# Optimization experiments

Hardware: AMD Instinct MI355X
Metric: run time of the kernel (lower is better)

The kernel has to match this reference:

```python
import jax, jax.numpy as jnp
import numpy as np

NUM_HEADS = 12
LN_EPS = 1e-5


def _ln(x, g, b):
    m = x.mean(-1, keepdims=True)
    v = ((x - m) ** 2).mean(-1, keepdims=True)
    return (x - m) * jax.lax.rsqrt(v + LN_EPS) * g + b


def _attn(q, k, v):
    sim = jnp.einsum('bid,bjd->bij', q, k)
    a = jax.nn.softmax(sim, axis=-1)
    return jnp.einsum('bij,bjd->bid', a, v)


def _var_attn(x, qkv_w, qkv_b, proj_w, proj_b, f, n, mode):
    # Faithful port of VarAttention.forward_features (num_tokens=0, pt_att=True)
    B, N, D = x.shape
    h = NUM_HEADS
    hd = D // h
    qkv = x @ qkv_w + qkv_b                       # [B, N, 3D]
    q, k, v = jnp.split(qkv, 3, axis=-1)

    def heads(t):  # 'b n (h d) -> (b h) n d'
        return t.reshape(B, N, h, hd).transpose(0, 2, 1, 3).reshape(B * h, N, hd)

    q = heads(q) * (hd ** -0.5)
    k = heads(k)
    v = heads(v)
    BH = B * h
    cls_q, q_ = q[:, :1], q[:, 1:]
    cls_k, k_ = k[:, :1], k[:, 1:]
    cls_v, v_ = v[:, :1], v[:, 1:]
    cls_out = _attn(cls_q, k, v)                  # cls attends over ALL tokens

    if mode == 'time':  # 'b (f n) d -> (b n) f d'
        to = lambda t: t.reshape(BH, f, n, hd).transpose(0, 2, 1, 3).reshape(BH * n, f, hd)
        back = lambda t: t.reshape(BH, n, f, hd).transpose(0, 2, 1, 3).reshape(BH, f * n, hd)
        r = n
    else:               # 'b (f n) d -> (b f) n d'
        to = lambda t: t.reshape(BH * f, n, hd)
        back = lambda t: t.reshape(BH, f * n, hd)
        r = f

    q_, k_, v_ = to(q_), to(k_), to(v_)
    cls_k_r = jnp.broadcast_to(cls_k[:, None], (BH, r, 1, hd)).reshape(BH * r, 1, hd)
    cls_v_r = jnp.broadcast_to(cls_v[:, None], (BH, r, 1, hd)).reshape(BH * r, 1, hd)
    out = _attn(q_, jnp.concatenate([cls_k_r, k_], axis=1),
                jnp.concatenate([cls_v_r, v_], axis=1))
    out = jnp.concatenate([cls_out, back(out)], axis=1)   # [(B h), N, d]
    out = out.reshape(B, h, N, hd).transpose(0, 2, 1, 3).reshape(B, N, D)
    return out @ proj_w + proj_b


def setup_inputs() -> dict:
    key = jax.random.key(0)
    ks = jax.random.split(key, 8)
    B, F, n, D = 8, 8, 196, 768
    N = 1 + F * n
    s = 0.02
    return {
        'x': jax.random.normal(ks[0], (B, N, D), jnp.float32),
        'norm1_g': jnp.ones((D,), jnp.float32), 'norm1_b': jnp.zeros((D,), jnp.float32),
        'norm2_g': jnp.ones((D,), jnp.float32), 'norm2_b': jnp.zeros((D,), jnp.float32),
        'norm3_g': jnp.ones((D,), jnp.float32), 'norm3_b': jnp.zeros((D,), jnp.float32),
        'attn_qkv_w': jax.random.normal(ks[1], (D, 3 * D), jnp.float32) * s,
        'attn_qkv_b': jnp.zeros((3 * D,), jnp.float32),
        'attn_proj_w': jax.random.normal(ks[2], (D, D), jnp.float32) * s,
        'attn_proj_b': jnp.zeros((D,), jnp.float32),
        'time_qkv_w': jax.random.normal(ks[3], (D, 3 * D), jnp.float32) * s,
        'time_qkv_b': jnp.zeros((3 * D,), jnp.float32),
        'time_proj_w': jax.random.normal(ks[4], (D, D), jnp.float32) * s,
        'time_proj_b': jnp.zeros((D,), jnp.float32),
        'fc1_w': jax.random.normal(ks[5], (D, 4 * D), jnp.float32) * s,
        'fc1_b': jnp.zeros((4 * D,), jnp.float32),
        'fc2_w': jax.random.normal(ks[6], (4 * D, D), jnp.float32) * s,
        'fc2_b': jnp.zeros((D,), jnp.float32),
        'f': 8,
    }


def reference(x, norm1_g, norm1_b, norm2_g, norm2_b, norm3_g, norm3_b,
              attn_qkv_w, attn_qkv_b, attn_proj_w, attn_proj_b,
              time_qkv_w, time_qkv_b, time_proj_w, time_proj_b,
              fc1_w, fc1_b, fc2_w, fc2_b, f):
    N = x.shape[1]
    n = (N - 1) // f  # patches per frame
    # divided time attention
    time_out = _var_attn(_ln(x, norm3_g, norm3_b), time_qkv_w, time_qkv_b,
                         time_proj_w, time_proj_b, f, n, 'time')
    time_residual = x + time_out
    # divided space attention (frozen-in-time: residual from original x)
    space_out = _var_attn(_ln(time_residual, norm1_g, norm1_b), attn_qkv_w, attn_qkv_b,
                          attn_proj_w, attn_proj_b, f, n, 'space')
    space_residual = x + space_out
    # MLP with exact GELU (torch nn.GELU default)
    h = jax.nn.gelu(_ln(space_residual, norm2_g, norm2_b) @ fc1_w + fc1_b, approximate=False)
    return space_residual + (h @ fc2_w + fc2_b)
```

## Files before the change

### kernel.cpp

```cpp
#include <hip/hip_runtime.h>
#include <hip/hip_bf16.h>
#include <math.h>

#define DM    768
#define NH    12
#define HD    64
#define BB    8
#define FF    8
#define NP    196
#define NT    1569
#define MROWS 12552
#define MPAD  12672
#define YT    99
#define QKVN  2304
#define FCN   3072
#define CHK   197

typedef short s16;
typedef __attribute__((ext_vector_type(8))) short short8;
typedef __attribute__((ext_vector_type(4))) float floatx4;

__device__ __forceinline__ float bf2f(s16 s) {
  union { unsigned u; float f; } x;
  x.u = ((unsigned)(unsigned short)s) << 16;
  return x.f;
}
__device__ __forceinline__ s16 f2bf(float f) {
  __hip_bfloat16 h = __float2bfloat16(f);
  s16 r;
  __builtin_memcpy(&r, &h, sizeof(r));
  return r;
}
__device__ __forceinline__ void gload16(const void* g, void* l) {
  __builtin_amdgcn_global_load_lds(
      (__attribute__((address_space(1))) void*)g,
      (__attribute__((address_space(3))) void*)l, 16, 0, 0);
}

__global__ void wtrans(const float* __restrict__ W, s16* __restrict__ Wt,
                       int K, int Nn) {
  __shared__ float t[32][33];
  int n0 = blockIdx.x * 32, k0 = blockIdx.y * 32;
  int tx = threadIdx.x, ty = threadIdx.y;
#pragma unroll
  for (int i = 0; i < 4; ++i)
    t[ty + 8*i][tx] = W[(size_t)(k0 + ty + 8*i) * Nn + n0 + tx];
  __syncthreads();
#pragma unroll
  for (int i = 0; i < 4; ++i)
    Wt[(size_t)(n0 + ty + 8*i) * K + k0 + tx] = f2bf(t[tx][ty + 8*i]);
}

__global__ __launch_bounds__(256) void ln_k(const float* __restrict__ in,
                                            const float* __restrict__ g,
                                            const float* __restrict__ b,
                                            s16* __restrict__ out) {
  __shared__ float red[8];
  int row = blockIdx.x;
  int tid = threadIdx.x;
  const float* rp = in + (size_t)row * DM;
  float v0 = rp[tid], v1 = rp[tid + 256], v2 = rp[tid + 512];
  float s = v0 + v1 + v2;
#pragma unroll
  for (int o = 32; o; o >>= 1) s += __shfl_down(s, o);
  if ((tid & 63) == 0) red[tid >> 6] = s;
  __syncthreads();
  float mean = (red[0] + red[1] + red[2] + red[3]) * (1.0f / DM);
  __syncthreads();
  float d0 = v0 - mean, d1 = v1 - mean, d2 = v2 - mean;
  float q = d0*d0 + d1*d1 + d2*d2;
#pragma unroll
  for (int o = 32; o; o >>= 1) q += __shfl_down(q, o);
  if ((tid & 63) == 0) red[tid >> 6] = q;
  __syncthreads();
  float var = (red[0] + red[1] + red[2] + red[3]) * (1.0f / DM);
  float rs = rsqrtf(var + 1e-5f);
  s16* op = out + (size_t)row * DM;
  op[tid      ] = f2bf(d0 * rs * g[tid      ] + b[tid      ]);
  op[tid + 256] = f2bf(d1 * rs * g[tid + 256] + b[tid + 256]);
  op[tid + 512] = f2bf(d2 * rs * g[tid + 512] + b[tid + 512]);
}

template<int EPI>
__global__ __launch_bounds__(256, 3) void gemm128(const s16* __restrict__ A,
                                                  const s16* __restrict__ Bt,
                                                  const float* __restrict__ bias,
                                                  const float* __restrict__ resid,
                                                  void* __restrict__ out,
                                                  int K, int Nn, int xt) {
  __shared__ s16 As0[128 * 32], As1[128 * 32];
  __shared__ s16 Bs0[128 * 32], Bs1[128 * 32];
  const int nwg = gridDim.x, orig = blockIdx.x;
  const int qq = nwg >> 3, rr = nwg & 7, xcd = orig & 7, lid = orig >> 3;
  const int wgid = (xcd < rr ? xcd * (qq + 1) : rr * (qq + 1) + (xcd - rr) * qq) + lid;
  const int row0 = (wgid / xt) * 128, col0 = (wgid % xt) * 128;
  const int tid = threadIdx.x;
  const int wave = tid >> 6, lane = tid & 63;
  const int wr = wave >> 1, wc = wave & 1;
  const int lrow = lane & 15, lk = (lane >> 4) * 8;

  floatx4 acc[4][4] = {};

  for (int k0 = 0; k0 < K; k0 += 64) {
#pragma unroll
    for (int i = 0; i < 2; ++i) {
      int elem = ((i * 4 + wave) << 9) + (lane << 3);
      int r = elem >> 5, c = elem & 31;
      const s16* Ap = A  + (size_t)(row0 + r) * K + k0 + c;
      const s16* Bp = Bt + (size_t)(col0 + r) * K + k0 + c;
      gload16(Ap,      As0 + elem);
      gload16(Ap + 32, As1 + elem);
      gload16(Bp,      Bs0 + elem);
      gload16(Bp + 32, Bs1 + elem);
    }
    __syncthreads();
    short8 af0[4], af1[4], bf0[4], bf1[4];
#pragma unroll
    for (int mi = 0; mi < 4; ++mi) {
      int ro = ((wr * 64 + mi * 16 + lrow) << 5) + lk;
      af0[mi] = *reinterpret_cast<const short8*>(As0 + ro);
      af1[mi] = *reinterpret_cast<const short8*>(As1 + ro);
    }
#pragma unroll
    for (int ni = 0; ni < 4; ++ni) {
      int ro = ((wc * 64 + ni * 16 + lrow) << 5) + lk;
      bf0[ni] = *reinterpret_cast<const short8*>(Bs0 + ro);
      bf1[ni] = *reinterpret_cast<const short8*>(Bs1 + ro);
    }
#pragma unroll
    for (int mi = 0; mi < 4; ++mi)
#pragma unroll
      for (int ni = 0; ni < 4; ++ni) {
        acc[mi][ni] = __builtin_amdgcn_mfma_f32_16x16x32_bf16(af0[mi], bf0[ni], acc[mi][ni], 0, 0, 0);
        acc[mi][ni] = __builtin_amdgcn_mfma_f32_16x16x32_bf16(af1[mi], bf1[ni], acc[mi][ni], 0, 0, 0);
      }
    __syncthreads();
  }

  const int c_lane = lane & 15, r_lane = lane >> 4;
#pragma unroll
  for (int mi = 0; mi < 4; ++mi) {
#pragma unroll
    for (int j = 0; j < 4; ++j) {
      int r = row0 + wr * 64 + mi * 16 + r_lane * 4 + j;
      if (r >= MROWS) continue;
#pragma unroll
      for (int ni = 0; ni < 4; ++ni) {
        int c = col0 + wc * 64 + ni * 16 + c_lane;
        float v = acc[mi][ni][j] + bias[c];
        size_t idx = (size_t)r * Nn + c;
        if (EPI == 0) {
          ((s16*)out)[idx] = f2bf(v);
        } else if (EPI == 1) {
          float ge = 0.5f * v * (1.0f + erff(v * 0.70710678118654752f));
          ((s16*)out)[idx] = f2bf(ge);
        } else {
          ((float*)out)[idx] = resid[idx] + v;
        }
      }
    }
  }
}

__global__ __launch_bounds__(256) void cls_part(const s16* __restrict__ qkv,
                                                float* __restrict__ part) {
  __shared__ float qs[64];
  __shared__ float sc[CHK];
  __shared__ float pacc[4][64];
  __shared__ float red[8];
  int blk = blockIdx.x; int ch = blk & 7; int bh = blk >> 3;
  int b = bh / NH, h = bh % NH;
  int tid = threadIdx.x;
  int t0 = ch * CHK;
  int nk = NT - t0; if (nk > CHK) nk = CHK;
  if (tid < 64) qs[tid] = 0.125f * bf2f(qkv[(size_t)(b*NT) * QKVN + h*HD + tid]);
  __syncthreads();
  for (int i = tid; i < nk; i += 256) {
    const s16* kp = qkv + (size_t)(b*NT + t0 + i) * QKVN + DM + h*HD;
    float dot = 0.f;
#pragma unroll
    for (int d8 = 0; d8 < 8; ++d8) {
      short8 kv = *reinterpret_cast<const short8*>(kp + d8*8);
#pragma unroll
      for (int j = 0; j < 8; ++j) dot += qs[d8*8 + j] * bf2f(kv[j]);
    }
    sc[i] = dot;
  }
  __syncthreads();
  float m = -1e30f;
  for (int i = tid; i < nk; i += 256) m = fmaxf(m, sc[i]);
#pragma unroll
  for (int o = 32; o; o >>= 1) m = fmaxf(m, __shfl_xor(m, o));
  if ((tid & 63) == 0) red[tid >> 6] = m;
  __syncthreads();
  m = fmaxf(fmaxf(red[0], red[1]), fmaxf(red[2], red[3]));
  __syncthreads();
  float s = 0.f;
  for (int i = tid; i < nk; i += 256) { float e = __expf(sc[i] - m); sc[i] = e; s += e; }
#pragma unroll
  for (int o = 32; o; o >>= 1) s += __shfl_xor(s, o);
  if ((tid & 63) == 0) red[tid >> 6] = s;
  __syncthreads();
  float S = red[0] + red[1] + red[2] + red[3];
  int d = tid & 63, pt = tid >> 6;
  float a = 0.f;
  for (int i = pt; i < nk; i += 4)
    a += sc[i] * bf2f(qkv[(size_t)(b*NT + t0 + i) * QKVN + 2*DM + h*HD + d]);
  pacc[pt][d] = a;
  __syncthreads();
  float* pp = part + (size_t)blk * 66;
  if (tid < 64) pp[2 + tid] = pacc[0][tid] + pacc[1][tid] + pacc[2][tid] + pacc[3][tid];
  if (tid == 0) { pp[0] = m; pp[1] = S; }
}

__global__ __launch_bounds__(64) void cls_combine(const float* __restrict__ part,
                                                  s16* __restrict__ aout) {
  int bh = blockIdx.x; int b = bh / NH, h = bh % NH;
  int d = threadIdx.x;
  float m = -1e30f;
#pragma unroll
  for (int c = 0; c < 8; ++c) m = fmaxf(m, part[(size_t)(bh*8 + c) * 66]);
  float S = 0.f, A = 0.f;
#pragma unroll
  for (int c = 0; c < 8; ++c) {
    const float* pp = part + (size_t)(bh*8 + c) * 66;
    float w = __expf(pp[0] - m);
    S += pp[1] * w;
    A += w * pp[2 + d];
  }
  aout[(size_t)(b*NT) * DM + h*HD + d] = f2bf(A / S);
}

__global__ __launch_bounds__(256) void time_attn(const s16* __restrict__ qkv,
                                                 s16* __restrict__ aout) {
  int g = blockIdx.x * 4 + (threadIdx.x >> 6);
  int lane = threadIdx.x & 63;
  int p = g % NP; int bh = g / NP; int b = bh / NH, h = bh % NH;
  int qi = lane >> 3;
  int dc = (lane & 7) * 8;
  int tokq = 1 + qi*NP + p;
  short8 qv = *reinterpret_cast<const short8*>(qkv + (size_t)(b*NT + tokq)*QKVN + h*HD + dc);
  float qf[8];
#pragma unroll
  for (int j = 0; j < 8; ++j) qf[j] = 0.125f * bf2f(qv[j]);
  float s[9];
#pragma unroll
  for (int kj = 0; kj < 9; ++kj) {
    int tok = (kj == 0) ? 0 : (1 + (kj - 1)*NP + p);
    short8 kv = *reinterpret_cast<const short8*>(qkv + (size_t)(b*NT + tok)*QKVN + DM + h*HD + dc);
    float d = 0.f;
#pragma unroll
    for (int j = 0; j < 8; ++j) d += qf[j] * bf2f(kv[j]);
    d += __shfl_xor(d, 1); d += __shfl_xor(d, 2); d += __shfl_xor(d, 4);
    s[kj] = d;
  }
  float m = s[0];
#pragma unroll
  for (int kj = 1; kj < 9; ++kj) m = fmaxf(m, s[kj]);
  float sum = 0.f;
#pragma unroll
  for (int kj = 0; kj < 9; ++kj) { s[kj] = expf(s[kj] - m); sum += s[kj]; }
  float inv = 1.0f / sum;
  float o[8] = {0,0,0,0,0,0,0,0};
#pragma unroll
  for (int kj = 0; kj < 9; ++kj) {
    int tok = (kj == 0) ? 0 : (1 + (kj - 1)*NP + p);
    short8 vv = *reinterpret_cast<const short8*>(qkv + (size_t)(b*NT + tok)*QKVN + 2*DM + h*HD + dc);
#pragma unroll
    for (int j = 0; j < 8; ++j) o[j] += s[kj] * bf2f(vv[j]);
  }
  short8 ov;
#pragma unroll
  for (int j = 0; j < 8; ++j) ov[j] = f2bf(o[j] * inv);
  *reinterpret_cast<short8*>(aout + (size_t)(b*NT + tokq)*DM + h*HD + dc) = ov;
}

#define PST 232
#define VST 232
__global__ __launch_bounds__(256) void space_attn_mfma(const s16* __restrict__ qkv,
                                                       s16* __restrict__ aout) {
  __shared__ s16 Vt[64][VST];
  __shared__ s16 P[4][16][PST];
  int grp = blockIdx.x;
  int fr = grp & 7; int bh = grp >> 3; int b = bh / NH, h = bh % NH;
  int tid = threadIdx.x, w = tid >> 6, lane = tid & 63;
  const size_t hbase = (size_t)(b * NT) * QKVN + h * HD;

  for (int idx = tid; idx < 224 * 8; idx += 256) {
    int kj = idx >> 3, c8 = idx & 7;
    if (kj < 197) {
      int tok = (kj == 0) ? 0 : (1 + fr * NP + kj - 1);
      short8 vv = *reinterpret_cast<const short8*>(qkv + hbase + (size_t)tok * QKVN + 2 * DM + c8 * 8);
#pragma unroll
      for (int j = 0; j < 8; ++j) Vt[c8 * 8 + j][kj] = vv[j];
    } else {
#pragma unroll
      for (int j = 0; j < 8; ++j) Vt[c8 * 8 + j][kj] = 0;
    }
  }
  for (int i = tid; i < 4 * 16 * 16; i += 256) {
    int wv = i >> 8, rr2 = (i >> 4) & 15, cc = i & 15;
    P[wv][rr2][208 + cc] = 0;
  }
  __syncthreads();

  const int lr = lane & 15, lg = lane >> 4;

  for (int t0 = w; t0 < 13; t0 += 4) {
    int q0 = t0 * 16;
    short8 aq[2];
#pragma unroll
    for (int c = 0; c < 2; ++c) {
      int tokq = 1 + fr * NP + q0 + lr;
      aq[c] = *reinterpret_cast<const short8*>(qkv + hbase + (size_t)tokq * QKVN + c * 32 + lg * 8);
    }
    short8 kb[13][2];
#pragma unroll
    for (int t = 0; t < 13; ++t) {
#pragma unroll
      for (int c = 0; c < 2; ++c) {
        int krow = t * 16 + lr;
        int tokk = (krow == 0) ? 0 : (1 + fr * NP + krow - 1);
        kb[t][c] = *reinterpret_cast<const short8*>(qkv + hbase + (size_t)tokk * QKVN + DM + c * 32 + lg * 8);
      }
    }
    floatx4 st[13];
#pragma unroll
    for (int t = 0; t < 13; ++t) st[t] = (floatx4){0.f, 0.f, 0.f, 0.f};
#pragma unroll
    for (int t = 0; t < 13; ++t) {
      st[t] = __builtin_amdgcn_mfma_f32_16x16x32_bf16(aq[0], kb[t][0], st[t], 0, 0, 0);
      st[t] = __builtin_amdgcn_mfma_f32_16x16x32_bf16(aq[1], kb[t][1], st[t], 0, 0, 0);
    }
    float mj[4] = {-1e30f, -1e30f, -1e30f, -1e30f};
#pragma unroll
    for (int t = 0; t < 13; ++t) {
      int key = t * 16 + lr;
#pragma unroll
      for (int j = 0; j < 4; ++j) {
        float v = (key < 197) ? st[t][j] * 0.125f : -1e30f;
        st[t][j] = v;
        mj[j] = fmaxf(mj[j], v);
      }
    }
#pragma unroll
    for (int j = 0; j < 4; ++j) {
      mj[j] = fmaxf(mj[j], __shfl_xor(mj[j], 1));
      mj[j] = fmaxf(mj[j], __shfl_xor(mj[j], 2));
      mj[j] = fmaxf(mj[j], __shfl_xor(mj[j], 4));
      mj[j] = fmaxf(mj[j], __shfl_xor(mj[j], 8));
    }
    float su[4] = {0.f, 0.f, 0.f, 0.f};
#pragma unroll
    for (int t = 0; t < 13; ++t)
#pragma unroll
      for (int j = 0; j < 4; ++j) {
        float e = __expf(st[t][j] - mj[j]);
        st[t][j] = e;
        su[j] += e;
      }
#pragma unroll
    for (int j = 0; j < 4; ++j) {
      su[j] += __shfl_xor(su[j], 1);
      su[j] += __shfl_xor(su[j], 2);
      su[j] += __shfl_xor(su[j], 4);
      su[j] += __shfl_xor(su[j], 8);
    }
    float inv[4];
#pragma unroll
    for (int j = 0; j < 4; ++j) inv[j] = 1.0f / su[j];
#pragma unroll
    for (int t = 0; t < 13; ++t)
#pragma unroll
      for (int j = 0; j < 4; ++j)
        P[w][lg * 4 + j][t * 16 + lr] = f2bf(st[t][j]);
    floatx4 o[4];
#pragma unroll
    for (int dt = 0; dt < 4; ++dt) o[dt] = (floatx4){0.f, 0.f, 0.f, 0.f};
#pragma unroll
    for (int kc = 0; kc < 7; ++kc) {
      short8 pa = *reinterpret_cast<const short8*>(&P[w][lr][kc * 32 + lg * 8]);
#pragma unroll
      for (int dt = 0; dt < 4; ++dt) {
        short8 vb = *reinterpret_cast<const short8*>(&Vt[dt * 16 + lr][kc * 32 + lg * 8]);
        o[dt] = __builtin_amdgcn_mfma_f32_16x16x32_bf16(pa, vb, o[dt], 0, 0, 0);
      }
    }
#pragma unroll
    for (int dt = 0; dt < 4; ++dt)
#pragma unroll
      for (int j = 0; j < 4; ++j) {
        int q = q0 + lg * 4 + j;
        if (q < NP) {
          int tokq = 1 + fr * NP + q;
          aout[(size_t)(b * NT + tokq) * DM + h * HD + dt * 16 + lr] = f2bf(o[dt][j] * inv[j]);
        }
      }
  }
}

extern "C" void kernel_launch(void* const* d_in, const int* in_sizes, int n_in,
                              void* d_out, int out_size, void* d_ws, size_t ws_size,
                              hipStream_t stream) {
  const float* x       = (const float*)d_in[0];
  const float* n1g     = (const float*)d_in[1];
  const float* n1b     = (const float*)d_in[2];
  const float* n2g     = (const float*)d_in[3];
  const float* n2b     = (const float*)d_in[4];
  const float* n3g     = (const float*)d_in[5];
  const float* n3b     = (const float*)d_in[6];
  const float* aqkv_w  = (const float*)d_in[7];
  const float* aqkv_b  = (const float*)d_in[8];
  const float* aproj_w = (const float*)d_in[9];
  const float* aproj_b = (const float*)d_in[10];
  const float* tqkv_w  = (const float*)d_in[11];
  const float* tqkv_b  = (const float*)d_in[12];
  const float* tproj_w = (const float*)d_in[13];
  const float* tproj_b = (const float*)d_in[14];
  const float* fc1_w   = (const float*)d_in[15];
  const float* fc1_b   = (const float*)d_in[16];
  const float* fc2_w   = (const float*)d_in[17];
  const float* fc2_b   = (const float*)d_in[18];
  float* out = (float*)d_out;

  char* ws = (char*)d_ws;
  size_t off = 0;
  auto alloc = [&](size_t bytes) -> void* {
    void* p = ws + off;
    off += (bytes + 255) & ~(size_t)255;
    return p;
  };
  s16*  wt_tqkv  = (s16*)alloc((size_t)QKVN * DM * 2);
  s16*  wt_tproj = (s16*)alloc((size_t)DM * DM * 2);
  s16*  wt_aqkv  = (s16*)alloc((size_t)QKVN * DM * 2);
  s16*  wt_aproj = (s16*)alloc((size_t)DM * DM * 2);
  s16*  wt_fc1   = (s16*)alloc((size_t)FCN * DM * 2);
  s16*  wt_fc2   = (s16*)alloc((size_t)DM * FCN * 2);
  s16*  ln_out   = (s16*)alloc((size_t)MPAD * DM * 2);
  s16*  attnout  = (s16*)alloc((size_t)MPAD * DM * 2);
  float* resid_s = (float*)alloc((size_t)MROWS * DM * 4);
  float* clspart = (float*)alloc((size_t)BB * NH * 8 * 66 * 4);
  char* big      = (char*)alloc((size_t)MPAD * FCN * 2);
  s16*   qkv_buf = (s16*)big;
  float* resid_t = (float*)big;
  s16*   h_buf   = (s16*)big;

  dim3 tb(32, 8);
  wtrans<<<dim3(QKVN/32, DM/32), tb, 0, stream>>>(tqkv_w,  wt_tqkv,  DM, QKVN);
  wtrans<<<dim3(DM/32,   DM/32), tb, 0, stream>>>(tproj_w, wt_tproj, DM, DM);
  wtrans<<<dim3(QKVN/32, DM/32), tb, 0, stream>>>(aqkv_w,  wt_aqkv,  DM, QKVN);
  wtrans<<<dim3(DM/32,   DM/32), tb, 0, stream>>>(aproj_w, wt_aproj, DM, DM);
  wtrans<<<dim3(FCN/32,  DM/32), tb, 0, stream>>>(fc1_w,   wt_fc1,   DM, FCN);
  wtrans<<<dim3(DM/32,  FCN/32), tb, 0, stream>>>(fc2_w,   wt_fc2,   FCN, DM);

  const int XT_QKV = QKVN / 128, XT_PRJ = DM / 128, XT_FC1 = FCN / 128;

  ln_k<<<MROWS, 256, 0, stream>>>(x, n3g, n3b, ln_out);
  gemm128<0><<<XT_QKV * YT, 256, 0, stream>>>(ln_out, wt_tqkv, tqkv_b, nullptr, qkv_buf, DM, QKVN, XT_QKV);
  cls_part<<<BB*NH*8, 256, 0, stream>>>(qkv_buf, clspart);
  cls_combine<<<BB*NH, 64, 0, stream>>>(clspart, attnout);
  time_attn<<<(BB*NH*NP)/4, 256, 0, stream>>>(qkv_buf, attnout);
  gemm128<2><<<XT_PRJ * YT, 256, 0, stream>>>(attnout, wt_tproj, tproj_b, x, resid_t, DM, DM, XT_PRJ);

  ln_k<<<MROWS, 256, 0, stream>>>(resid_t, n1g, n1b, ln_out);
  gemm128<0><<<XT_QKV * YT, 256, 0, stream>>>(ln_out, wt_aqkv, aqkv_b, nullptr, qkv_buf, DM, QKVN, XT_QKV);
  cls_part<<<BB*NH*8, 256, 0, stream>>>(qkv_buf, clspart);
  cls_combine<<<BB*NH, 64, 0, stream>>>(clspart, attnout);
  space_attn_mfma<<<BB*NH*FF, 256, 0, stream>>>(qkv_buf, attnout);
  gemm128<2><<<XT_PRJ * YT, 256, 0, stream>>>(attnout, wt_aproj, aproj_b, x, resid_s, DM, DM, XT_PRJ);

  ln_k<<<MROWS, 256, 0, stream>>>(resid_s, n2g, n2b, ln_out);
  gemm128<1><<<XT_FC1 * YT, 256, 0, stream>>>(ln_out, wt_fc1, fc1_b, nullptr, h_buf, DM, FCN, XT_FC1);
  gemm128<2><<<XT_PRJ * YT, 256, 0, stream>>>(h_buf, wt_fc2, fc2_b, resid_s, out, FCN, DM, XT_PRJ);
}
```

Measured before the change: 651.5 us.

## Double-buffer GEMM shared memory tiles to overlap global loads with MFMA

The bf16 GEMM kernel now keeps two LDS stages and issues the global-to-LDS loads for the next K tile before computing on the current one, with one barrier per iteration. This is meant to hide global load latency behind the MFMA work. LDS per block doubles to 64KB and launch bounds drop from 3 to 2 blocks per CU, so occupancy falls. Whether the loads actually overlap depends on how gload16 waits on completion.

```diff
diff --git a/kernel.cpp b/kernel.cpp
--- a/kernel.cpp
+++ b/kernel.cpp
@@ -82,14 +82,14 @@
 }
 
 template<int EPI>
-__global__ __launch_bounds__(256, 3) void gemm128(const s16* __restrict__ A,
+__global__ __launch_bounds__(256, 2) void gemm128(const s16* __restrict__ A,
                                                   const s16* __restrict__ Bt,
                                                   const float* __restrict__ bias,
                                                   const float* __restrict__ resid,
                                                   void* __restrict__ out,
                                                   int K, int Nn, int xt) {
-  __shared__ s16 As0[128 * 32], As1[128 * 32];
-  __shared__ s16 Bs0[128 * 32], Bs1[128 * 32];
+  __shared__ s16 As[2][2][128 * 32];
+  __shared__ s16 Bs[2][2][128 * 32];
   const int nwg = gridDim.x, orig = blockIdx.x;
   const int qq = nwg >> 3, rr = nwg & 7, xcd = orig & 7, lid = orig >> 3;
   const int wgid = (xcd < rr ? xcd * (qq + 1) : rr * (qq + 1) + (xcd - rr) * qq) + lid;
@@ -98,34 +98,44 @@
   const int wave = tid >> 6, lane = tid & 63;
   const int wr = wave >> 1, wc = wave & 1;
   const int lrow = lane & 15, lk = (lane >> 4) * 8;
+  const int nt = K >> 6;
+
+#define STAGE(kt_, cur_)                                                       \
+  {                                                                            \
+    int k0s = (kt_) * 64;                                                      \
+    _Pragma("unroll")                                                          \
+    for (int i = 0; i < 2; ++i) {                                              \
+      int elem = ((i * 4 + wave) << 9) + (lane << 3);                          \
+      int r = elem >> 5, c = elem & 31;                                        \
+      const s16* Ap = A  + (size_t)(row0 + r) * K + k0s + c;                   \
+      const s16* Bp = Bt + (size_t)(col0 + r) * K + k0s + c;                   \
+      gload16(Ap,      As[cur_][0] + elem);                                    \
+      gload16(Ap + 32, As[cur_][1] + elem);                                    \
+      gload16(Bp,      Bs[cur_][0] + elem);                                    \
+      gload16(Bp + 32, Bs[cur_][1] + elem);                                    \
+    }                                                                          \
+  }
 
   floatx4 acc[4][4] = {};
 
-  for (int k0 = 0; k0 < K; k0 += 64) {
-#pragma unroll
-    for (int i = 0; i < 2; ++i) {
-      int elem = ((i * 4 + wave) << 9) + (lane << 3);
-      int r = elem >> 5, c = elem & 31;
-      const s16* Ap = A  + (size_t)(row0 + r) * K + k0 + c;
-      const s16* Bp = Bt + (size_t)(col0 + r) * K + k0 + c;
-      gload16(Ap,      As0 + elem);
-      gload16(Ap + 32, As1 + elem);
-      gload16(Bp,      Bs0 + elem);
-      gload16(Bp + 32, Bs1 + elem);
-    }
-    __syncthreads();
+  STAGE(0, 0)
+  __syncthreads();
+
+  int cur = 0;
+  for (int kt = 0; kt < nt; ++kt) {
+    if (kt + 1 < nt) STAGE(kt + 1, cur ^ 1)
     short8 af0[4], af1[4], bf0[4], bf1[4];
 #pragma unroll
     for (int mi = 0; mi < 4; ++mi) {
       int ro = ((wr * 64 + mi * 16 + lrow) << 5) + lk;
-      af0[mi] = *reinterpret_cast<const short8*>(As0 + ro);
-      af1[mi] = *reinterpret_cast<const short8*>(As1 + ro);
+      af0[mi] = *reinterpret_cast<const short8*>(As[cur][0] + ro);
+      af1[mi] = *reinterpret_cast<const short8*>(As[cur][1] + ro);
     }
 #pragma unroll
     for (int ni = 0; ni < 4; ++ni) {
       int ro = ((wc * 64 + ni * 16 + lrow) << 5) + lk;
-      bf0[ni] = *reinterpret_cast<const short8*>(Bs0 + ro);
-      bf1[ni] = *reinterpret_cast<const short8*>(Bs1 + ro);
+      bf0[ni] = *reinterpret_cast<const short8*>(Bs[cur][0] + ro);
+      bf1[ni] = *reinterpret_cast<const short8*>(Bs[cur][1] + ro);
     }
 #pragma unroll
     for (int mi = 0; mi < 4; ++mi)
@@ -135,7 +145,9 @@
         acc[mi][ni] = __builtin_amdgcn_mfma_f32_16x16x32_bf16(af1[mi], bf1[ni], acc[mi][ni], 0, 0, 0);
       }
     __syncthreads();
-  }
+    cur ^= 1;
+  }
+#undef STAGE
 
   const int c_lane = lane & 15, r_lane = lane >> 4;
 #pragma unroll
```

Result: slower. 797.8 us (+22.5%).
